# Kernel tuning notes

Hardware: AMD Instinct MI355X
Metric: run time of the kernel (lower is better)

The kernel has to match this reference:

```python
import jax, jax.numpy as jnp
import numpy as np

LN_EPS = 1e-5


def setup_inputs() -> dict:
    key = jax.random.key(0)
    ks = jax.random.split(key, 8)
    B, N, M, D = 4, 512, 512, 256
    s = 1.0 / np.sqrt(D)
    return {
        "x": jax.random.normal(ks[0], (B, N, D), jnp.float32),
        "c": jax.random.normal(ks[1], (B, M, D), jnp.float32),
        "mask": jnp.ones((B, N, M), jnp.float32),
        "Wq": jax.random.normal(ks[2], (D, D), jnp.float32) * s,
        "bq": jax.random.normal(ks[3], (D,), jnp.float32) * s,
        "Wk": jax.random.normal(ks[4], (D, D), jnp.float32) * s,
        "Wr": jax.random.normal(ks[5], (D,), jnp.float32) * s,
        "Wv": jax.random.normal(ks[6], (D, D), jnp.float32) * s,
        "bv": jax.random.normal(ks[7], (D,), jnp.float32) * s,
        "gamma": jnp.ones((D,), jnp.float32),
        "beta": jnp.zeros((D,), jnp.float32),
    }


def reference(x, c, mask, Wq, bq, Wk, Wr, Wv, bv, gamma, beta):
    D = x.shape[-1]
    deflator = 1.0 / jnp.sqrt(jnp.asarray(D, x.dtype))
    # q: (B, n, 1, d), k: (B, 1, m, d) -- Bahdanau-style additive scores
    q = jnp.tanh(jnp.einsum("bnd,ed->bne", x, Wq) + bq)[:, :, None, :]
    k = jnp.tanh(jnp.einsum("bmd,ed->bme", c, Wk))[:, None, :, :]
    # weight_reduce to scalar score, tanh then relu, squeeze last dim
    w = jax.nn.relu(jnp.tanh(jnp.einsum("bnmd,d->bnm", q + k, Wr)))
    w = w * mask
    v = (jnp.einsum("bmd,ed->bme", c, Wv) + bv) * deflator
    add = jnp.einsum("bnm,bmd->bnd", w, v)
    h = x + add
    mu = jnp.mean(h, axis=-1, keepdims=True)
    var = jnp.mean(jnp.square(h - mu), axis=-1, keepdims=True)
    return (h - mu) / jnp.sqrt(var + LN_EPS) * gamma + beta
```

## Files before the change

kernel.cpp:

```cpp
#include <hip/hip_runtime.h>
#include <math.h>

#define BB 4
#define NN 512
#define MM 512
#define DD 256

typedef short  s16x8 __attribute__((ext_vector_type(8)));
typedef __bf16 bf16x8 __attribute__((ext_vector_type(8)));
typedef float  f32x4 __attribute__((ext_vector_type(4)));
typedef unsigned short u16x4 __attribute__((ext_vector_type(4)));

static __device__ __forceinline__ f32x4 mfma16(s16x8 a, s16x8 b, f32x4 c) {
    return __builtin_amdgcn_mfma_f32_16x16x32_bf16(
        __builtin_bit_cast(bf16x8, a), __builtin_bit_cast(bf16x8, b), c, 0, 0, 0);
}

static __device__ __forceinline__ unsigned short f2b(float f) {
    union { float f; unsigned u; } v; v.f = f;
    unsigned r = v.u + 0x7FFFu + ((v.u >> 16) & 1u);
    return (unsigned short)(r >> 16);
}

static __device__ __forceinline__ s16x8 cvt8(const float* __restrict__ p) {
    const float4 a = *(const float4*)p;
    const float4 b = *(const float4*)(p + 4);
    s16x8 r;
    r[0] = (short)f2b(a.x); r[1] = (short)f2b(a.y);
    r[2] = (short)f2b(a.z); r[3] = (short)f2b(a.w);
    r[4] = (short)f2b(b.x); r[5] = (short)f2b(b.y);
    r[6] = (short)f2b(b.z); r[7] = (short)f2b(b.w);
    return r;
}

__global__ __launch_bounds__(256) void k_proj(
    const float* __restrict__ x, const float* __restrict__ c,
    const float* __restrict__ Wq, const float* __restrict__ bq,
    const float* __restrict__ Wk, const float* __restrict__ Wr,
    const float* __restrict__ Wv, const float* __restrict__ bv,
    float* __restrict__ qs, float* __restrict__ ks,
    unsigned short* __restrict__ vT)
{
    __shared__ float red[4][16];
    const int tid  = threadIdx.x;
    const int lane = tid & 63, w = tid >> 6;
    const int li   = lane & 15, g = lane >> 4;
    const bool isk = blockIdx.x >= 128;
    const int row0 = (blockIdx.x & 127) << 4;
    const float* __restrict__ src = isk ? c : x;

    const float* ap = src + (size_t)(row0 + li) * DD + g * 8;
    s16x8 af[8];
    #pragma unroll
    for (int kk = 0; kk < 8; ++kk) af[kk] = cvt8(ap + kk * 32);

    const int e_base = w * 64 + li;

    if (!isk) {
        f32x4 acc[4];
        const float* bp[4];
        #pragma unroll
        for (int nt = 0; nt < 4; ++nt) {
            acc[nt] = (f32x4){0.f, 0.f, 0.f, 0.f};
            bp[nt] = Wq + (size_t)(e_base + nt * 16) * DD + g * 8;
        }
        #pragma unroll
        for (int kk = 0; kk < 8; ++kk)
            #pragma unroll
            for (int nt = 0; nt < 4; ++nt)
                acc[nt] = mfma16(af[kk], cvt8(bp[nt] + kk * 32), acc[nt]);

        float p[4] = {0.f, 0.f, 0.f, 0.f};
        #pragma unroll
        for (int nt = 0; nt < 4; ++nt) {
            const int e = e_base + nt * 16;
            const float bqe = bq[e], wre = Wr[e];
            #pragma unroll
            for (int r = 0; r < 4; ++r)
                p[r] += wre * tanhf(acc[nt][r] + bqe);
        }
        #pragma unroll
        for (int r = 0; r < 4; ++r) {
            p[r] += __shfl_xor(p[r], 1);
            p[r] += __shfl_xor(p[r], 2);
            p[r] += __shfl_xor(p[r], 4);
            p[r] += __shfl_xor(p[r], 8);
        }
        if (li == 0) {
            #pragma unroll
            for (int r = 0; r < 4; ++r) red[w][g * 4 + r] = p[r];
        }
        __syncthreads();
        if (tid < 16)
            qs[row0 + tid] = red[0][tid] + red[1][tid] + red[2][tid] + red[3][tid];
    } else {
        f32x4 ak[4], av[4];
        const float* bpk[4];
        const float* bpv[4];
        #pragma unroll
        for (int nt = 0; nt < 4; ++nt) {
            ak[nt] = (f32x4){0.f, 0.f, 0.f, 0.f};
            av[nt] = (f32x4){0.f, 0.f, 0.f, 0.f};
            bpk[nt] = Wk + (size_t)(e_base + nt * 16) * DD + g * 8;
            bpv[nt] = Wv + (size_t)(e_base + nt * 16) * DD + g * 8;
        }
        #pragma unroll
        for (int kk = 0; kk < 8; ++kk)
            #pragma unroll
            for (int nt = 0; nt < 4; ++nt) {
                ak[nt] = mfma16(af[kk], cvt8(bpk[nt] + kk * 32), ak[nt]);
                av[nt] = mfma16(af[kk], cvt8(bpv[nt] + kk * 32), av[nt]);
            }

        const int b  = row0 >> 9;
        const int m0 = row0 & 511;
        unsigned short* vTb = vT + (size_t)b * (DD * MM);
        #pragma unroll
        for (int nt = 0; nt < 4; ++nt) {
            const int e = e_base + nt * 16;
            const float bve = bv[e];
            u16x4 o;
            #pragma unroll
            for (int r = 0; r < 4; ++r)
                o[r] = f2b((av[nt][r] + bve) * 0.0625f);
            *(u16x4*)(vTb + (size_t)e * MM + m0 + g * 4) = o;
        }

        float p[4] = {0.f, 0.f, 0.f, 0.f};
        #pragma unroll
        for (int nt = 0; nt < 4; ++nt) {
            const int e = e_base + nt * 16;
            const float wre = Wr[e];
            #pragma unroll
            for (int r = 0; r < 4; ++r)
                p[r] += wre * tanhf(ak[nt][r]);
        }
        #pragma unroll
        for (int r = 0; r < 4; ++r) {
            p[r] += __shfl_xor(p[r], 1);
            p[r] += __shfl_xor(p[r], 2);
            p[r] += __shfl_xor(p[r], 4);
            p[r] += __shfl_xor(p[r], 8);
        }
        if (li == 0) {
            #pragma unroll
            for (int r = 0; r < 4; ++r) red[w][g * 4 + r] = p[r];
        }
        __syncthreads();
        if (tid < 16)
            ks[row0 + tid] = red[0][tid] + red[1][tid] + red[2][tid] + red[3][tid];
    }
}

__global__ __launch_bounds__(256) void k_main(
    const float* __restrict__ x, const float* __restrict__ mask,
    const float* __restrict__ qs, const float* __restrict__ ks,
    const unsigned short* __restrict__ vT,
    const float* __restrict__ gamma, const float* __restrict__ beta,
    float* __restrict__ out)
{
    __shared__ unsigned short w_lds[16][512];
    __shared__ float ksm[MM];
    __shared__ float h_lds[16][264];
    const int tid  = threadIdx.x;
    const int lane = tid & 63, w = tid >> 6;
    const int li   = lane & 15, g = lane >> 4;
    const int n0g  = blockIdx.x << 3;
    const int b    = n0g >> 9;

    ksm[tid]       = ks[(b << 9) + tid];
    ksm[tid + 256] = ks[(b << 9) + 256 + tid];
    __syncthreads();

    char* wbase = (char*)w_lds;
    const float* __restrict__ mrow = mask + (size_t)n0g * MM;
    #pragma unroll
    for (int it = 0; it < 16; ++it) {
        const int i = it >> 1;
        const int m = ((it & 1) << 8) + tid;
        const float qv = qs[n0g + i];
        float s = fmaxf(tanhf(qv + ksm[m]), 0.f) * mrow[(size_t)i * MM + m];
        *(unsigned short*)(wbase + (i << 10) + ((m << 1) ^ ((i & 7) << 4))) = f2b(s);
    }
    __syncthreads();

    f32x4 acc[4];
    const unsigned short* vp[4];
    #pragma unroll
    for (int nt = 0; nt < 4; ++nt) {
        acc[nt] = (f32x4){0.f, 0.f, 0.f, 0.f};
        vp[nt] = vT + (size_t)b * (DD * MM)
                    + (size_t)(w * 64 + nt * 16 + li) * MM + g * 8;
    }
    const char* arow = wbase + (li << 10);
    const int aswz = (li & 7) << 4;
    #pragma unroll
    for (int kk = 0; kk < 16; ++kk) {
        const s16x8 a = *(const s16x8*)(arow + (((kk << 6) + (g << 4)) ^ aswz));
        #pragma unroll
        for (int nt = 0; nt < 4; ++nt)
            acc[nt] = mfma16(a, *(const s16x8*)(vp[nt] + kk * 32), acc[nt]);
    }

    #pragma unroll
    for (int nt = 0; nt < 4; ++nt) {
        const int e = w * 64 + nt * 16 + li;
        #pragma unroll
        for (int r = 0; r < 4; ++r)
            h_lds[g * 4 + r][e] = acc[nt][r];
    }
    __syncthreads();

    const float4 gm = ((const float4*)gamma)[lane];
    const float4 bt = ((const float4*)beta)[lane];
    #pragma unroll
    for (int rr = 0; rr < 2; ++rr) {
        const int row = (w << 1) + rr;
        const float4 hv = *(const float4*)&h_lds[row][lane << 2];
        const float4 xv = *(const float4*)(x + ((size_t)(n0g + row)) * DD + (lane << 2));
        float4 h;
        h.x = xv.x + hv.x; h.y = xv.y + hv.y;
        h.z = xv.z + hv.z; h.w = xv.w + hv.w;
        float s  = h.x + h.y + h.z + h.w;
        float s2 = h.x * h.x + h.y * h.y + h.z * h.z + h.w * h.w;
        #pragma unroll
        for (int off = 32; off; off >>= 1) {
            s  += __shfl_xor(s, off);
            s2 += __shfl_xor(s2, off);
        }
        const float mean = s * (1.0f / DD);
        const float var  = s2 * (1.0f / DD) - mean * mean;
        const float inv  = rsqrtf(var + 1e-5f);
        float4 o;
        o.x = (h.x - mean) * inv * gm.x + bt.x;
        o.y = (h.y - mean) * inv * gm.y + bt.y;
        o.z = (h.z - mean) * inv * gm.z + bt.z;
        o.w = (h.w - mean) * inv * gm.w + bt.w;
        *(float4*)(out + ((size_t)(n0g + row)) * DD + (lane << 2)) = o;
    }
}

extern "C" void kernel_launch(void* const* d_in, const int* in_sizes, int n_in,
                              void* d_out, int out_size, void* d_ws, size_t ws_size,
                              hipStream_t stream) {
    const float* x     = (const float*)d_in[0];
    const float* c     = (const float*)d_in[1];
    const float* mask  = (const float*)d_in[2];
    const float* Wq    = (const float*)d_in[3];
    const float* bq    = (const float*)d_in[4];
    const float* Wk    = (const float*)d_in[5];
    const float* Wr    = (const float*)d_in[6];
    const float* Wv    = (const float*)d_in[7];
    const float* bv    = (const float*)d_in[8];
    const float* gamma = (const float*)d_in[9];
    const float* beta  = (const float*)d_in[10];
    float* out = (float*)d_out;

    float* ws = (float*)d_ws;
    float* qs  = ws;
    float* ksb = ws + 2048;
    unsigned short* vT = (unsigned short*)(ws + 4096);

    k_proj<<<256, 256, 0, stream>>>(x, c, Wq, bq, Wk, Wr, Wv, bv, qs, ksb, vT);
    k_main<<<256, 256, 0, stream>>>(x, mask, qs, ksb, vT, gamma, beta, out);
}
```

Before: 38.54 us.

## Split projection and attention work across twice as many blocks with partial sums

The projection kernel now splits the output-feature dimension into two halves per row tile. Each half writes a partial q/k score, and the main kernel sums the two partials when it loads them. The main kernel now handles 4 query rows per block instead of 8, which doubles both grids to 512 blocks so every CU gets more than one block. The score computation is also vectorized to four elements per thread, using float4 loads of mask and k. In exchange, each block reloads the full V tile for fewer rows, and wasted MFMA rows increase.

```diff
diff --git a/kernel.cpp b/kernel.cpp
--- a/kernel.cpp
+++ b/kernel.cpp
@@ -38,15 +38,17 @@
     const float* __restrict__ Wq, const float* __restrict__ bq,
     const float* __restrict__ Wk, const float* __restrict__ Wr,
     const float* __restrict__ Wv, const float* __restrict__ bv,
-    float* __restrict__ qs, float* __restrict__ ks,
+    float* __restrict__ qp, float* __restrict__ kp,
     unsigned short* __restrict__ vT)
 {
     __shared__ float red[4][16];
     const int tid  = threadIdx.x;
     const int lane = tid & 63, w = tid >> 6;
     const int li   = lane & 15, g = lane >> 4;
-    const bool isk = blockIdx.x >= 128;
-    const int row0 = (blockIdx.x & 127) << 4;
+    const bool isk = blockIdx.x >= 256;
+    const int idx  = blockIdx.x & 255;
+    const int row0 = (idx >> 1) << 4;
+    const int eh   = idx & 1;
     const float* __restrict__ src = isk ? c : x;
 
     const float* ap = src + (size_t)(row0 + li) * DD + g * 8;
@@ -54,25 +56,25 @@
     #pragma unroll
     for (int kk = 0; kk < 8; ++kk) af[kk] = cvt8(ap + kk * 32);
 
-    const int e_base = w * 64 + li;
+    const int e_base = eh * 128 + w * 32 + li;
 
     if (!isk) {
-        f32x4 acc[4];
-        const float* bp[4];
-        #pragma unroll
-        for (int nt = 0; nt < 4; ++nt) {
+        f32x4 acc[2];
+        const float* bp[2];
+        #pragma unroll
+        for (int nt = 0; nt < 2; ++nt) {
             acc[nt] = (f32x4){0.f, 0.f, 0.f, 0.f};
             bp[nt] = Wq + (size_t)(e_base + nt * 16) * DD + g * 8;
         }
         #pragma unroll
         for (int kk = 0; kk < 8; ++kk)
             #pragma unroll
-            for (int nt = 0; nt < 4; ++nt)
+            for (int nt = 0; nt < 2; ++nt)
                 acc[nt] = mfma16(af[kk], cvt8(bp[nt] + kk * 32), acc[nt]);
 
         float p[4] = {0.f, 0.f, 0.f, 0.f};
         #pragma unroll
-        for (int nt = 0; nt < 4; ++nt) {
+        for (int nt = 0; nt < 2; ++nt) {
             const int e = e_base + nt * 16;
             const float bqe = bq[e], wre = Wr[e];
             #pragma unroll
@@ -92,13 +94,14 @@
         }
         __syncthreads();
         if (tid < 16)
-            qs[row0 + tid] = red[0][tid] + red[1][tid] + red[2][tid] + red[3][tid];
+            qp[((row0 + tid) << 1) + eh] =
+                red[0][tid] + red[1][tid] + red[2][tid] + red[3][tid];
     } else {
-        f32x4 ak[4], av[4];
-        const float* bpk[4];
-        const float* bpv[4];
-        #pragma unroll
-        for (int nt = 0; nt < 4; ++nt) {
+        f32x4 ak[2], av[2];
+        const float* bpk[2];
+        const float* bpv[2];
+        #pragma unroll
+        for (int nt = 0; nt < 2; ++nt) {
             ak[nt] = (f32x4){0.f, 0.f, 0.f, 0.f};
             av[nt] = (f32x4){0.f, 0.f, 0.f, 0.f};
             bpk[nt] = Wk + (size_t)(e_base + nt * 16) * DD + g * 8;
@@ -107,7 +110,7 @@
         #pragma unroll
         for (int kk = 0; kk < 8; ++kk)
             #pragma unroll
-            for (int nt = 0; nt < 4; ++nt) {
+            for (int nt = 0; nt < 2; ++nt) {
                 ak[nt] = mfma16(af[kk], cvt8(bpk[nt] + kk * 32), ak[nt]);
                 av[nt] = mfma16(af[kk], cvt8(bpv[nt] + kk * 32), av[nt]);
             }
@@ -116,7 +119,7 @@
         const int m0 = row0 & 511;
         unsigned short* vTb = vT + (size_t)b * (DD * MM);
         #pragma unroll
-        for (int nt = 0; nt < 4; ++nt) {
+        for (int nt = 0; nt < 2; ++nt) {
             const int e = e_base + nt * 16;
             const float bve = bv[e];
             u16x4 o;
@@ -128,7 +131,7 @@
 
         float p[4] = {0.f, 0.f, 0.f, 0.f};
         #pragma unroll
-        for (int nt = 0; nt < 4; ++nt) {
+        for (int nt = 0; nt < 2; ++nt) {
             const int e = e_base + nt * 16;
             const float wre = Wr[e];
             #pragma unroll
@@ -148,13 +151,14 @@
         }
         __syncthreads();
         if (tid < 16)
-            ks[row0 + tid] = red[0][tid] + red[1][tid] + red[2][tid] + red[3][tid];
+            kp[((row0 + tid) << 1) + eh] =
+                red[0][tid] + red[1][tid] + red[2][tid] + red[3][tid];
     }
 }
 
 __global__ __launch_bounds__(256) void k_main(
     const float* __restrict__ x, const float* __restrict__ mask,
-    const float* __restrict__ qs, const float* __restrict__ ks,
+    const float* __restrict__ qp, const float* __restrict__ kp,
     const unsigned short* __restrict__ vT,
     const float* __restrict__ gamma, const float* __restrict__ beta,
     float* __restrict__ out)
@@ -165,22 +169,36 @@
     const int tid  = threadIdx.x;
     const int lane = tid & 63, w = tid >> 6;
     const int li   = lane & 15, g = lane >> 4;
-    const int n0g  = blockIdx.x << 3;
+    const int n0g  = blockIdx.x << 2;
     const int b    = n0g >> 9;
 
-    ksm[tid]       = ks[(b << 9) + tid];
-    ksm[tid + 256] = ks[(b << 9) + 256 + tid];
+    const float2* __restrict__ kp2 = (const float2*)kp + (b << 9);
+    {
+        const float2 a0 = kp2[tid];
+        const float2 a1 = kp2[tid + 256];
+        ksm[tid]       = a0.x + a0.y;
+        ksm[tid + 256] = a1.x + a1.y;
+    }
     __syncthreads();
 
     char* wbase = (char*)w_lds;
     const float* __restrict__ mrow = mask + (size_t)n0g * MM;
-    #pragma unroll
-    for (int it = 0; it < 16; ++it) {
-        const int i = it >> 1;
-        const int m = ((it & 1) << 8) + tid;
-        const float qv = qs[n0g + i];
-        float s = fmaxf(tanhf(qv + ksm[m]), 0.f) * mrow[(size_t)i * MM + m];
-        *(unsigned short*)(wbase + (i << 10) + ((m << 1) ^ ((i & 7) << 4))) = f2b(s);
+    const float2* __restrict__ qp2 = (const float2*)qp;
+    #pragma unroll
+    for (int it = 0; it < 2; ++it) {
+        const int L = (it << 10) + (tid << 2);
+        const int i = L >> 9;
+        const int m = L & 511;
+        const float2 qv2 = qp2[n0g + i];
+        const float qv = qv2.x + qv2.y;
+        const float4 mk = *(const float4*)(mrow + (size_t)i * MM + m);
+        const float4 kv = *(const float4*)&ksm[m];
+        u16x4 o;
+        o[0] = f2b(fmaxf(tanhf(qv + kv.x), 0.f) * mk.x);
+        o[1] = f2b(fmaxf(tanhf(qv + kv.y), 0.f) * mk.y);
+        o[2] = f2b(fmaxf(tanhf(qv + kv.z), 0.f) * mk.z);
+        o[3] = f2b(fmaxf(tanhf(qv + kv.w), 0.f) * mk.w);
+        *(u16x4*)(wbase + (i << 10) + ((m << 1) ^ ((i & 7) << 4))) = o;
     }
     __syncthreads();
 
@@ -211,11 +229,10 @@
     }
     __syncthreads();
 
-    const float4 gm = ((const float4*)gamma)[lane];
-    const float4 bt = ((const float4*)beta)[lane];
-    #pragma unroll
-    for (int rr = 0; rr < 2; ++rr) {
-        const int row = (w << 1) + rr;
+    {
+        const int row = w;
+        const float4 gm = ((const float4*)gamma)[lane];
+        const float4 bt = ((const float4*)beta)[lane];
         const float4 hv = *(const float4*)&h_lds[row][lane << 2];
         const float4 xv = *(const float4*)(x + ((size_t)(n0g + row)) * DD + (lane << 2));
         float4 h;
@@ -257,10 +274,10 @@
     float* out = (float*)d_out;
 
     float* ws = (float*)d_ws;
-    float* qs  = ws;
-    float* ksb = ws + 2048;
-    unsigned short* vT = (unsigned short*)(ws + 4096);
-
-    k_proj<<<256, 256, 0, stream>>>(x, c, Wq, bq, Wk, Wr, Wv, bv, qs, ksb, vT);
-    k_main<<<256, 256, 0, stream>>>(x, mask, qs, ksb, vT, gamma, beta, out);
-}
+    float* qp = ws;
+    float* kp = ws + 4096;
+    unsigned short* vT = (unsigned short*)(ws + 8192);
+
+    k_proj<<<512, 256, 0, stream>>>(x, c, Wq, bq, Wk, Wr, Wv, bv, qp, kp, vT);
+    k_main<<<512, 256, 0, stream>>>(x, mask, qp, kp, vT, gamma, beta, out);
+}
```

Result: slower. 41.22 us (+7.0%).
